# Performance work log

Measured on AMD Instinct MI355X. Metric: run time of the kernel, lower is better.

The kernel has to match this reference:

```python
import jax, jax.numpy as jnp
import numpy as np

B, T, D, H, O = 4096, 512, 18, 8, 1


def setup_inputs() -> dict:
    key = jax.random.key(0)
    ks = jax.random.split(key, 8)
    x = jax.random.normal(ks[0], (B, T, D), dtype=jnp.float32)
    # PackedSequence invariant: lengths sorted descending, each >= 1
    lengths = jax.random.randint(ks[1], (B,), 1, T + 1, dtype=jnp.int32)
    lengths = jnp.sort(lengths)[::-1]
    s = 1.0 / np.sqrt(H)
    W_ih = jax.random.uniform(ks[2], (4 * H, D), jnp.float32, -s, s)
    W_hh = jax.random.uniform(ks[3], (4 * H, H), jnp.float32, -s, s)
    b_ih = jax.random.uniform(ks[4], (4 * H,), jnp.float32, -s, s)
    b_hh = jax.random.uniform(ks[5], (4 * H,), jnp.float32, -s, s)
    W_lin = jax.random.uniform(ks[6], (O, H), jnp.float32, -s, s)
    b_lin = jax.random.uniform(ks[7], (O,), jnp.float32, -s, s)
    return {"x": x, "lengths": lengths, "W_ih": W_ih, "W_hh": W_hh,
            "b_ih": b_ih, "b_hh": b_hh, "W_lin": W_lin, "b_lin": b_lin}


def reference(x, lengths, W_ih, W_hh, b_ih, b_hh, W_lin, b_lin):
    # Single-layer LSTM over ragged (packed) sequences, zero init hidden,
    # then a Linear head on every valid timestep (squash_packed).
    bias = b_ih + b_hh  # [4H]
    xg = jnp.einsum('btd,gd->btg', x, W_ih) + bias  # precompute input gates [B,T,4H]
    xg_t = jnp.swapaxes(xg, 0, 1)  # [T,B,4H]
    # mask[t,b] = t < lengths[b]  (packed steps actually computed)
    mask = (jnp.arange(T)[:, None] < lengths[None, :])[..., None]  # [T,B,1]

    h0 = jnp.zeros((B, H), x.dtype)
    c0 = jnp.zeros((B, H), x.dtype)

    def step(carry, inp):
        h, c = carry
        g_x, m = inp  # [B,4H], [B,1]
        gates = g_x + h @ W_hh.T
        i, f, g, o = jnp.split(gates, 4, axis=-1)  # torch gate order i,f,g,o
        i = jax.nn.sigmoid(i); f = jax.nn.sigmoid(f); o = jax.nn.sigmoid(o)
        g = jnp.tanh(g)
        c_new = f * c + i * g
        h_new = o * jnp.tanh(c_new)
        # beyond a sequence's length the packed LSTM never updates its state
        h = jnp.where(m, h_new, h)
        c = jnp.where(m, c_new, c)
        return (h, c), jnp.where(m, h_new, 0.0)

    (_, _), hs = jax.lax.scan(step, (h0, c0), (xg_t, mask))  # hs: [T,B,H]
    hs = jnp.swapaxes(hs, 0, 1)  # [B,T,H]
    y = jnp.einsum('bth,oh->bto', hs, W_lin) + b_lin  # [B,T,O]
    # linear head only applied to valid (packed) entries; zero out padding
    pad_mask = jnp.swapaxes(mask, 0, 1)  # [B,T,1]
    return jnp.where(pad_mask, y, 0.0)
```

## Files before the change

### kernel.cpp

```cpp
#include <hip/hip_runtime.h>


namespace {

constexpr int NT = 512;
constexpr int ND = 18;
constexpr float LOG2E = 1.4426950408889634f;

typedef float v2f __attribute__((ext_vector_type(2)));
typedef float v4f __attribute__((ext_vector_type(4)));

template <int C>
__device__ __forceinline__ float fdpp(float v) {
    const int i = __float_as_int(v);
    return __int_as_float(__builtin_amdgcn_update_dpp(i, i, C, 0xF, 0xF, true));
}
__device__ __forceinline__ void gload_lds(const void* g, void* l) {
    __builtin_amdgcn_global_load_lds(
        (const __attribute__((address_space(1))) void*)g,
        (__attribute__((address_space(3))) void*)l, 4, 0, 0);
}

__global__ __launch_bounds__(128, 1) void lstm_pc(
    const float* __restrict__ x, const int* __restrict__ lengths,
    const float* __restrict__ W_ih, const float* __restrict__ W_hh,
    const float* __restrict__ b_ih, const float* __restrict__ b_hh,
    const float* __restrict__ W_lin, const float* __restrict__ b_lin,
    float* __restrict__ out)
{
    __shared__ __align__(16) float Aring[32][4][16];
    __shared__ __align__(16) float Bring[4][8][4][2];
    __shared__ __align__(16) v2f   XG[4][8][16][5];

    const int q_ = (int)blockIdx.x & 255;
    const int r_ = (int)blockIdx.x >> 8;
    const int g  = (r_ == 0) ? q_ : (r_ == 1) ? (1023 - q_)
                 : (r_ == 2) ? (256 + q_) : (767 - q_);

    const int tid  = (int)threadIdx.x;
    const int wav  = tid >> 6;
    const int w    = tid & 63;
    const int grp  = w >> 4;
    const int l16  = w & 15;
    const int p    = l16 >> 3;
    const int j    = l16 & 7;
    const int lenmax = lengths[g * 4];
    const int nwin = (lenmax + 15) >> 4;
    const int rowA = j + (p ? 8 : 0);
    const int rowB = j + (p ? 24 : 16);

    if (wav == 1) {
        v2f wxA[9], wxB[9];
        {
            const v2f* ra = (const v2f*)(W_ih + rowA * ND);
            const v2f* rb = (const v2f*)(W_ih + rowB * ND);
#pragma unroll
            for (int k = 0; k < 9; ++k) { wxA[k] = ra[k]; wxB[k] = rb[k]; }
        }
        const float biasA = b_ih[rowA] + b_hh[rowA];
        const float biasB = b_ih[rowB] + b_hh[rowB];

        const char* xc = (const char*)x;
        const char* pA = xc + (size_t)((((unsigned)(g * 4 + (w >> 4)) * (NT * ND))
                                       + (unsigned)(w & 15)) * 4u);
        const char* pB = xc + (size_t)((((unsigned)(g * 4 + ((w >> 1) & 3)) * (NT * ND))
                                       + 16u + (unsigned)(w & 1)) * 4u);
        const unsigned rB0 = (unsigned)(w >> 3);

        auto dma_chunk = [&](int dd) {
            const int r0 = dd * 8;
#pragma unroll
            for (int k = 0; k < 8; ++k) {
                const int rr = (r0 + k < NT) ? (r0 + k) : (NT - 1);
                gload_lds(pA + (unsigned)rr * 72u, &Aring[(r0 + k) & 31][0][0]);
            }
            unsigned rb = (unsigned)r0 + rB0;
            rb = (rb < (unsigned)NT) ? rb : (unsigned)(NT - 1);
            gload_lds(pB + rb * 72u, &Bring[dd & 3][0][0][0]);
        };

        auto produce_chunk = [&](int cc) {
            const int s0 = (cc * 8) & 31;
            const int bf = cc & 3;
#pragma unroll
            for (int k = 0; k < 8; ++k) {
                const v4f* ap = (const v4f*)&Aring[s0 + k][grp][0];
                const v4f q0 = ap[0], q1 = ap[1], q2 = ap[2], q3 = ap[3];
                const v2f bt = *(const v2f*)&Bring[bf][k][grp][0];
                v2f aA = v2f{biasA, 0.f}, aB = v2f{biasB, 0.f};
                aA = q0.lo * wxA[0] + aA;  aB = q0.lo * wxB[0] + aB;
                aA = q0.hi * wxA[1] + aA;  aB = q0.hi * wxB[1] + aB;
                aA = q1.lo * wxA[2] + aA;  aB = q1.lo * wxB[2] + aB;
                aA = q1.hi * wxA[3] + aA;  aB = q1.hi * wxB[3] + aB;
                aA = q2.lo * wxA[4] + aA;  aB = q2.lo * wxB[4] + aB;
                aA = q2.hi * wxA[5] + aA;  aB = q2.hi * wxB[5] + aB;
                aA = q3.lo * wxA[6] + aA;  aB = q3.lo * wxB[6] + aB;
                aA = q3.hi * wxA[7] + aA;  aB = q3.hi * wxB[7] + aB;
                aA = bt * wxA[8] + aA;     aB = bt * wxB[8] + aB;
                XG[bf][k][l16][grp] = v2f{aA.x + aA.y, aB.x + aB.y};
            }
        };

        dma_chunk(0); dma_chunk(1); dma_chunk(2); dma_chunk(3);
        asm volatile("s_waitcnt vmcnt(18)" ::: "memory");
        produce_chunk(0);
        produce_chunk(1);
        asm volatile("s_waitcnt lgkmcnt(0)" ::: "memory");
        __builtin_amdgcn_sched_barrier(0);
        __builtin_amdgcn_s_barrier();
        __builtin_amdgcn_sched_barrier(0);

        for (int I = 0; I < nwin; ++I) {
            dma_chunk(2 * I + 4);
            dma_chunk(2 * I + 5);
            asm volatile("s_waitcnt vmcnt(18)" ::: "memory");
            produce_chunk(2 * I + 2);
            produce_chunk(2 * I + 3);
            asm volatile("s_waitcnt lgkmcnt(0)" ::: "memory");
            __builtin_amdgcn_sched_barrier(0);
            __builtin_amdgcn_s_barrier();
            __builtin_amdgcn_sched_barrier(0);
        }
    } else {
        const int len = lengths[g * 4 + grp];

        int idx[8];
        idx[0] = j;
        idx[1] = __builtin_amdgcn_update_dpp(0, j, 0x121, 0xF, 0xF, true) & 7;
        idx[2] = __builtin_amdgcn_update_dpp(0, j, 0x122, 0xF, 0xF, true) & 7;
        idx[3] = __builtin_amdgcn_update_dpp(0, j, 0x123, 0xF, 0xF, true) & 7;
        idx[4] = __builtin_amdgcn_update_dpp(0, j, 0x124, 0xF, 0xF, true) & 7;
        idx[5] = __builtin_amdgcn_update_dpp(0, j, 0x125, 0xF, 0xF, true) & 7;
        idx[6] = __builtin_amdgcn_update_dpp(0, j, 0x126, 0xF, 0xF, true) & 7;
        idx[7] = __builtin_amdgcn_update_dpp(0, j, 0x127, 0xF, 0xF, true) & 7;

        v2f whA[4], whB[4], wl2[4];
#pragma unroll
        for (int r = 0; r < 4; ++r) {
            whA[r] = v2f{W_hh[rowA * 8 + idx[2 * r]], W_hh[rowA * 8 + idx[2 * r + 1]]};
            whB[r] = v2f{W_hh[rowB * 8 + idx[2 * r]], W_hh[rowB * 8 + idx[2 * r + 1]]};
            wl2[r] = v2f{W_lin[idx[2 * r]], W_lin[idx[2 * r + 1]]};
        }
        const float bl = b_lin[0];
        const float Kp = p ? -LOG2E : -2.0f * LOG2E;

        float* yb = out + (size_t)(g * 4 + grp) * NT;

        v2f hp[4] = {v2f{0.f, 0.f}, v2f{0.f, 0.f}, v2f{0.f, 0.f}, v2f{0.f, 0.f}};
        float c_ = 0.0f, hown = 0.0f;

        __builtin_amdgcn_s_barrier();
        __builtin_amdgcn_sched_barrier(0);

        for (int I = 0; I < nwin; ++I) {
            const int t = I * 16;
            const v2f* xg0 = &XG[(2 * I) & 3][0][l16][grp];
            const v2f* xg1 = &XG[(2 * I + 1) & 3][0][l16][grp];
            float y[16];
            v2f xgn = xg0[0];
#pragma unroll
            for (int k = 0; k < 16; ++k) {
                const v2f xgc = xgn;
                if (k < 15) xgn = (k + 1 < 8) ? xg0[(k + 1) * 80] : xg1[(k + 1 - 8) * 80];

                v2f tA = hp[0] * whA[0];
                tA = hp[1] * whA[1] + tA;
                tA = hp[2] * whA[2] + tA;
                tA = hp[3] * whA[3] + tA;
                v2f tB = hp[0] * whB[0];
                tB = hp[1] * whB[1] + tB;
                tB = hp[2] * whB[2] + tB;
                tB = hp[3] * whB[3] + tB;
                const float aA = (xgc.x + tA.x) + tA.y;
                const float aB = (xgc.y + tB.x) + tB.y;

                const float vA = __builtin_amdgcn_rcpf(
                    1.0f + __builtin_amdgcn_exp2f(aA * -LOG2E));
                const float sB = __builtin_amdgcn_rcpf(
                    1.0f + __builtin_amdgcn_exp2f(aB * Kp));
                const float vB = p ? sB : fmaf(2.0f, sB, -1.0f);

                const float send1 = p ? vA : (vA * vB);
                const float ex1 = fdpp<0x128>(send1);
                const float f_ = p ? send1 : ex1;
                const float ig_ = p ? ex1 : send1;
                c_ = fmaf(f_, c_, ig_);
                const float tc = fmaf(-2.0f, __builtin_amdgcn_rcpf(
                    1.0f + __builtin_amdgcn_exp2f(c_ * (2.0f * LOG2E))), 1.0f);
                const float ex2 = fdpp<0x128>(vB);
                const float o_ = p ? vB : ex2;
                hown = o_ * tc;

                const float h1 = fdpp<0x121>(hown);
                const float h2 = fdpp<0x122>(hown);
                const float h3 = fdpp<0x123>(hown);
                const float h4 = fdpp<0x124>(hown);
                const float h5 = fdpp<0x125>(hown);
                const float h6 = fdpp<0x126>(hown);
                const float h7 = fdpp<0x127>(hown);
                hp[0] = v2f{hown, h1}; hp[1] = v2f{h2, h3};
                hp[2] = v2f{h4, h5};   hp[3] = v2f{h6, h7};

                v2f ya = hp[0] * wl2[0];
                ya = hp[1] * wl2[1] + ya;
                ya = hp[2] * wl2[2] + ya;
                ya = hp[3] * wl2[3] + ya;
                y[k] = (ya.x + ya.y) + bl;
            }

            if (l16 == 0) {
                if (t + 15 < len) {
                    *(v4f*)(yb + t)      = v4f{y[0],  y[1],  y[2],  y[3]};
                    *(v4f*)(yb + t + 4)  = v4f{y[4],  y[5],  y[6],  y[7]};
                    *(v4f*)(yb + t + 8)  = v4f{y[8],  y[9],  y[10], y[11]};
                    *(v4f*)(yb + t + 12) = v4f{y[12], y[13], y[14], y[15]};
                } else {
#pragma unroll
                    for (int k = 0; k < 16; ++k)
                        if (t + k < len) yb[t + k] = y[k];
                }
            }
            __builtin_amdgcn_sched_barrier(0);
            __builtin_amdgcn_s_barrier();
            __builtin_amdgcn_sched_barrier(0);
        }
    }
}

}

extern "C" void kernel_launch(void* const* d_in, const int* in_sizes, int n_in,
                              void* d_out, int out_size, void* d_ws, size_t ws_size,
                              hipStream_t stream) {
    const float* x     = (const float*)d_in[0];
    const int*   lens  = (const int*)d_in[1];
    const float* W_ih  = (const float*)d_in[2];
    const float* W_hh  = (const float*)d_in[3];
    const float* b_ih  = (const float*)d_in[4];
    const float* b_hh  = (const float*)d_in[5];
    const float* W_lin = (const float*)d_in[6];
    const float* b_lin = (const float*)d_in[7];
    float* out = (float*)d_out;

    hipMemsetAsync(out, 0, (size_t)4096 * NT * sizeof(float), stream);

    lstm_pc<<<1024, 128, 0, stream>>>(x, lens, W_ih, W_hh, b_ih, b_hh,
                                      W_lin, b_lin, out);
}
```

Baseline: 75.95 us.

## Move linear head off recurrence wave into producer wave via LDS h buffer

Result: slower. 77.51 us (+2.1%).

```diff
diff --git a/kernel.cpp b/kernel.cpp
--- a/kernel.cpp
+++ b/kernel.cpp
@@ -31,6 +31,7 @@
     __shared__ __align__(16) float Aring[32][4][16];
     __shared__ __align__(16) float Bring[4][8][4][2];
     __shared__ __align__(16) v2f   XG[4][8][16][5];
+    __shared__ __align__(16) float Hbuf[2][4][16][8];
 
     const int q_ = (int)blockIdx.x & 255;
     const int r_ = (int)blockIdx.x >> 8;
@@ -59,6 +60,14 @@
         }
         const float biasA = b_ih[rowA] + b_hh[rowA];
         const float biasB = b_ih[rowB] + b_hh[rowB];
+
+        float wl[8];
+#pragma unroll
+        for (int k = 0; k < 8; ++k) wl[k] = W_lin[k];
+        const float bl = b_lin[0];
+        const int sH = w >> 4, kH = w & 15;
+        const int lenH = lengths[g * 4 + sH];
+        float* yH = out + (size_t)(g * 4 + sH) * NT + kH;
 
         const char* xc = (const char*)x;
         const char* pA = xc + (size_t)((((unsigned)(g * 4 + (w >> 4)) * (NT * ND))
@@ -101,6 +110,22 @@
             }
         };
 
+        auto head_win = [&](int W) {
+            const v4f* hq = (const v4f*)&Hbuf[W & 1][sH][kH][0];
+            const v4f h0 = hq[0], h1 = hq[1];
+            float yv = bl;
+            yv = fmaf(h0.x, wl[0], yv);
+            yv = fmaf(h0.y, wl[1], yv);
+            yv = fmaf(h0.z, wl[2], yv);
+            yv = fmaf(h0.w, wl[3], yv);
+            yv = fmaf(h1.x, wl[4], yv);
+            yv = fmaf(h1.y, wl[5], yv);
+            yv = fmaf(h1.z, wl[6], yv);
+            yv = fmaf(h1.w, wl[7], yv);
+            const int t = W * 16 + kH;
+            if (t < lenH) yH[W * 16] = yv;
+        };
+
         dma_chunk(0); dma_chunk(1); dma_chunk(2); dma_chunk(3);
         asm volatile("s_waitcnt vmcnt(18)" ::: "memory");
         produce_chunk(0);
@@ -113,17 +138,17 @@
         for (int I = 0; I < nwin; ++I) {
             dma_chunk(2 * I + 4);
             dma_chunk(2 * I + 5);
-            asm volatile("s_waitcnt vmcnt(18)" ::: "memory");
+            asm volatile("s_waitcnt vmcnt(36)" ::: "memory");
             produce_chunk(2 * I + 2);
             produce_chunk(2 * I + 3);
+            if (I > 0) head_win(I - 1);
             asm volatile("s_waitcnt lgkmcnt(0)" ::: "memory");
             __builtin_amdgcn_sched_barrier(0);
             __builtin_amdgcn_s_barrier();
             __builtin_amdgcn_sched_barrier(0);
         }
+        head_win(nwin - 1);
     } else {
-        const int len = lengths[g * 4 + grp];
-
         int idx[8];
         idx[0] = j;
         idx[1] = __builtin_amdgcn_update_dpp(0, j, 0x121, 0xF, 0xF, true) & 7;
@@ -134,17 +159,13 @@
         idx[6] = __builtin_amdgcn_update_dpp(0, j, 0x126, 0xF, 0xF, true) & 7;
         idx[7] = __builtin_amdgcn_update_dpp(0, j, 0x127, 0xF, 0xF, true) & 7;
 
-        v2f whA[4], whB[4], wl2[4];
+        v2f whA[4], whB[4];
 #pragma unroll
         for (int r = 0; r < 4; ++r) {
             whA[r] = v2f{W_hh[rowA * 8 + idx[2 * r]], W_hh[rowA * 8 + idx[2 * r + 1]]};
             whB[r] = v2f{W_hh[rowB * 8 + idx[2 * r]], W_hh[rowB * 8 + idx[2 * r + 1]]};
-            wl2[r] = v2f{W_lin[idx[2 * r]], W_lin[idx[2 * r + 1]]};
-        }
-        const float bl = b_lin[0];
+        }
         const float Kp = p ? -LOG2E : -2.0f * LOG2E;
-
-        float* yb = out + (size_t)(g * 4 + grp) * NT;
 
         v2f hp[4] = {v2f{0.f, 0.f}, v2f{0.f, 0.f}, v2f{0.f, 0.f}, v2f{0.f, 0.f}};
         float c_ = 0.0f, hown = 0.0f;
@@ -153,10 +174,9 @@
         __builtin_amdgcn_sched_barrier(0);
 
         for (int I = 0; I < nwin; ++I) {
-            const int t = I * 16;
             const v2f* xg0 = &XG[(2 * I) & 3][0][l16][grp];
             const v2f* xg1 = &XG[(2 * I + 1) & 3][0][l16][grp];
-            float y[16];
+            float* hw = &Hbuf[I & 1][grp][0][j];
             v2f xgn = xg0[0];
 #pragma unroll
             for (int k = 0; k < 16; ++k) {
@@ -191,6 +211,8 @@
                 const float o_ = p ? vB : ex2;
                 hown = o_ * tc;
 
+                hw[k * 8] = hown;
+
                 const float h1 = fdpp<0x121>(hown);
                 const float h2 = fdpp<0x122>(hown);
                 const float h3 = fdpp<0x123>(hown);
@@ -200,26 +222,9 @@
                 const float h7 = fdpp<0x127>(hown);
                 hp[0] = v2f{hown, h1}; hp[1] = v2f{h2, h3};
                 hp[2] = v2f{h4, h5};   hp[3] = v2f{h6, h7};
-
-                v2f ya = hp[0] * wl2[0];
-                ya = hp[1] * wl2[1] + ya;
-                ya = hp[2] * wl2[2] + ya;
-                ya = hp[3] * wl2[3] + ya;
-                y[k] = (ya.x + ya.y) + bl;
             }
 
-            if (l16 == 0) {
-                if (t + 15 < len) {
-                    *(v4f*)(yb + t)      = v4f{y[0],  y[1],  y[2],  y[3]};
-                    *(v4f*)(yb + t + 4)  = v4f{y[4],  y[5],  y[6],  y[7]};
-                    *(v4f*)(yb + t + 8)  = v4f{y[8],  y[9],  y[10], y[11]};
-                    *(v4f*)(yb + t + 12) = v4f{y[12], y[13], y[14], y[15]};
-                } else {
-#pragma unroll
-                    for (int k = 0; k < 16; ++k)
-                        if (t + k < len) yb[t + k] = y[k];
-                }
-            }
+            asm volatile("s_waitcnt lgkmcnt(0)" ::: "memory");
             __builtin_amdgcn_sched_barrier(0);
             __builtin_amdgcn_s_barrier();
             __builtin_amdgcn_sched_barrier(0);
```
